# Kernel optimization log

Measured on AMD Instinct MI355X. Metric: run time of the kernel, lower is better.

## Reference

```python
import jax, jax.numpy as jnp
import numpy as np

B, L, D = 2, 2048, 1024
H = 16
HD = D // H  # 64


def _orthogonal_projection(key, d, m):
    g = jax.random.normal(key, (d, m), dtype=jnp.float32)
    q, r = jnp.linalg.qr(g)
    s = jnp.sign(jnp.diagonal(r))
    s = jnp.where(s == 0, 1.0, s)
    q = q * s[None, :]
    # preserve_variance=True
    return q * np.sqrt(d / m)


def setup_inputs() -> dict:
    key = jax.random.key(0)
    ks = jax.random.split(key, 8)
    x = jax.random.normal(ks[0], (B, L, D), dtype=jnp.float32)
    p = jax.random.normal(ks[1], (B, L, D), dtype=jnp.float32)
    s = 1.0 / np.sqrt(D)
    W_qkv = jax.random.uniform(ks[2], (3 * D, D), dtype=jnp.float32, minval=-s, maxval=s)
    b_qkv = jax.random.uniform(ks[3], (3 * D,), dtype=jnp.float32, minval=-s, maxval=s)
    W_out = jax.random.uniform(ks[4], (D, D), dtype=jnp.float32, minval=-s, maxval=s)
    b_out = jax.random.uniform(ks[5], (D,), dtype=jnp.float32, minval=-s, maxval=s)
    proj = _orthogonal_projection(ks[6], D, D // 2)
    return {"x": x, "p": p, "W_qkv": W_qkv, "b_qkv": b_qkv,
            "W_out": W_out, "b_out": b_out, "proj": proj}


def reference(x, p, W_qkv, b_qkv, W_out, b_out, proj):
    # QKV projection: (B,L,D) -> (B,L,3,H,HD)
    qkv = (jnp.einsum('bld,ed->ble', x, W_qkv) + b_qkv).reshape(B, L, 3, H, HD)
    q, k, v = qkv[:, :, 0], qkv[:, :, 1], qkv[:, :, 2]

    # Collaborative rotary phases from conditioning tokens: (B,L,H,HD/2)
    phases = (p @ proj).reshape(B, L, H, HD // 2)  # phase_scale = 1.0
    cos, sin = jnp.cos(phases), jnp.sin(phases)

    half = HD // 2
    # non-interleaved rotary: split head_dim into two halves
    def rot(t):
        t1, t2 = t[..., :half], t[..., half:]
        return jnp.concatenate([t1 * cos - t2 * sin, t1 * sin + t2 * cos], axis=-1)

    q, k = rot(q), rot(k)

    scale = HD ** -0.5
    scores = jnp.einsum('bqhd,bkhd->bhqk', q, k) * scale
    attn = jax.nn.softmax(scores, axis=-1)
    out = jnp.einsum('bhqk,bkhd->bqhd', attn, v).reshape(B, L, D)
    return jnp.einsum('bld,ed->ble', out, W_out) + b_out
```

## Files before the change

### kernel.cpp

```cpp
#include <hip/hip_runtime.h>
#include <hip/hip_bf16.h>
#include <math.h>

namespace {
constexpr int Bb = 2;
constexpr int Ll = 2048;
constexpr int Dd = 1024;
constexpr int Hh = 16;
constexpr int NT = Bb * Ll;
constexpr int D3 = 3 * Dd;
constexpr int PH = Dd / 2;
constexpr int LDK = 72;
}

typedef __attribute__((ext_vector_type(8))) short bf16x8;
typedef __attribute__((ext_vector_type(4))) float f32x4;

__device__ inline unsigned pack2bf(float a, float b) {
  __hip_bfloat162 t = __float22bfloat162_rn(float2{a, b});
  union { __hip_bfloat162 h; unsigned u; } cv; cv.h = t;
  return cv.u;
}

__device__ inline float bfhalf(unsigned u, int hi) {
  union { unsigned u; float f; } c;
  c.u = hi ? (u & 0xffff0000u) : (u << 16);
  return c.f;
}

__device__ inline void async_cp16(const void* gsrc, void* ldst) {
  __builtin_amdgcn_global_load_lds(
      (const __attribute__((address_space(1))) unsigned int*)gsrc,
      (__attribute__((address_space(3))) unsigned int*)ldst, 16, 0, 0);
}

__global__ __launch_bounds__(256) void prep_kernel(
    const float4* __restrict__ p, uint2* __restrict__ p_hi4, uint2* __restrict__ p_lo4,
    const float* __restrict__ proj, short* __restrict__ th, short* __restrict__ tl,
    const float4* __restrict__ x, const float4* __restrict__ wq, const float4* __restrict__ wo,
    uint2* __restrict__ xd, uint2* __restrict__ wqd, uint2* __restrict__ wod)
{
  __shared__ float Ls[64][65];
  const int bid = blockIdx.x;
  const int tid = threadIdx.x;

  if (bid < 4096) {
    const int i = bid * 256 + tid;
    const float4 f = p[i];
    float hf[4], lf[4];
    const float ff[4] = {f.x, f.y, f.z, f.w};
#pragma unroll
    for (int j = 0; j < 4; ++j) {
      const __hip_bfloat16 h = __float2bfloat16(ff[j]);
      hf[j] = __bfloat162float(h);
      lf[j] = ff[j] - hf[j];
    }
    p_hi4[i] = make_uint2(pack2bf(hf[0], hf[1]), pack2bf(hf[2], hf[3]));
    p_lo4[i] = make_uint2(pack2bf(lf[0], lf[1]), pack2bf(lf[2], lf[3]));
  } else if (bid < 4224) {
    const int bx = bid - 4096;
    const int d0 = (bx & 15) * 64, m0 = (bx >> 4) * 64;
    const int r = tid >> 4, c4 = (tid & 15) * 4;
#pragma unroll
    for (int it = 0; it < 4; ++it) {
      const int row = it * 16 + r;
      const float4 v = *(const float4*)&proj[(size_t)(d0 + row) * PH + m0 + c4];
      Ls[row][c4] = v.x; Ls[row][c4+1] = v.y; Ls[row][c4+2] = v.z; Ls[row][c4+3] = v.w;
    }
    __syncthreads();
#pragma unroll
    for (int it = 0; it < 4; ++it) {
      const int row = it * 16 + r;
      float hf[4], lf[4];
#pragma unroll
      for (int j = 0; j < 4; ++j) {
        const float v = Ls[c4 + j][row];
        const __hip_bfloat16 h = __float2bfloat16(v);
        hf[j] = __bfloat162float(h);
        lf[j] = v - hf[j];
      }
      *(uint2*)&th[(size_t)(m0 + row) * Dd + d0 + c4] = make_uint2(pack2bf(hf[0], hf[1]), pack2bf(hf[2], hf[3]));
      *(uint2*)&tl[(size_t)(m0 + row) * Dd + d0 + c4] = make_uint2(pack2bf(lf[0], lf[1]), pack2bf(lf[2], lf[3]));
    }
  } else {
    int i = (bid - 4224) * 256 + tid;
    const float4* s; uint2* d;
    if (i < 1048576) { s = x; d = xd; }
    else if (i < 1048576 + 786432) { i -= 1048576; s = wq; d = wqd; }
    else { i -= 1048576 + 786432; s = wo; d = wod; }
    const float4 f = s[i];
    d[i] = make_uint2(pack2bf(f.x, f.y), pack2bf(f.z, f.w));
  }
}

__global__ __launch_bounds__(256) void gemm_nn_split(
    const short* __restrict__ Ah_g, const short* __restrict__ Al_g,
    const short* __restrict__ Wh_g, const short* __restrict__ Wl_g,
    float* __restrict__ C)
{
  __shared__ __align__(16) short Ah[64 * 32], Al[64 * 32], Wh[64 * 32], Wl[64 * 32];
  const int tid = threadIdx.x;
  const int w = tid >> 6, lane = tid & 63;
  const int l15 = lane & 15, quad = lane >> 4;
  const int n0 = blockIdx.y * 64, m0 = blockIdx.x * 64;

  const int row = tid >> 2, cc = tid & 3;
  const int ksw = (cc ^ (row & 3)) * 8;
  const short* gAh = Ah_g + (size_t)(n0 + row) * Dd + ksw;
  const short* gAl = Al_g + (size_t)(n0 + row) * Dd + ksw;
  const short* gWh = Wh_g + (size_t)(m0 + row) * Dd + ksw;
  const short* gWl = Wl_g + (size_t)(m0 + row) * Dd + ksw;
  short* lAh = Ah + tid * 8;
  short* lAl = Al + tid * 8;
  short* lWh = Wh + tid * 8;
  short* lWl = Wl + tid * 8;

  f32x4 acc[4];
#pragma unroll
  for (int j = 0; j < 4; ++j) acc[j] = f32x4{0.f, 0.f, 0.f, 0.f};

  const int swq = (quad ^ (l15 & 3)) * 8;

  for (int k0 = 0; k0 < Dd; k0 += 32) {
    __syncthreads();
    async_cp16(gAh + k0, lAh);
    async_cp16(gAl + k0, lAl);
    async_cp16(gWh + k0, lWh);
    async_cp16(gWl + k0, lWl);
    __syncthreads();

    bf16x8 ah, al, wh[4], wl[4];
    ah = *(const bf16x8*)&Ah[(w * 16 + l15) * 32 + swq];
    al = *(const bf16x8*)&Al[(w * 16 + l15) * 32 + swq];
#pragma unroll
    for (int j = 0; j < 4; ++j) {
      wh[j] = *(const bf16x8*)&Wh[(j * 16 + l15) * 32 + swq];
      wl[j] = *(const bf16x8*)&Wl[(j * 16 + l15) * 32 + swq];
    }
#pragma unroll
    for (int j = 0; j < 4; ++j) {
      acc[j] = __builtin_amdgcn_mfma_f32_16x16x32_bf16(ah, wh[j], acc[j], 0, 0, 0);
      acc[j] = __builtin_amdgcn_mfma_f32_16x16x32_bf16(ah, wl[j], acc[j], 0, 0, 0);
      acc[j] = __builtin_amdgcn_mfma_f32_16x16x32_bf16(al, wh[j], acc[j], 0, 0, 0);
    }
  }

#pragma unroll
  for (int r = 0; r < 4; ++r) {
    float* crow = C + (size_t)(n0 + w * 16 + quad * 4 + r) * PH + m0 + l15;
#pragma unroll
    for (int j = 0; j < 4; ++j) crow[j * 16] = acc[j][r];
  }
}

__global__ __launch_bounds__(256) void gemm_qkv_fused(
    const __hip_bfloat16* __restrict__ A, const __hip_bfloat16* __restrict__ W,
    const float* __restrict__ bias, const float* __restrict__ phases,
    __hip_bfloat16* __restrict__ q_bf, __hip_bfloat16* __restrict__ k_bf,
    __hip_bfloat16* __restrict__ vt_g)
{
  __shared__ __align__(16) short As[128 * 32];
  __shared__ __align__(16) short Ws[128 * 32];
  const int tid = threadIdx.x;
  const int w = tid >> 6, lane = tid & 63;
  const int l15 = lane & 15, quad = lane >> 4;
  const int wn = w >> 1, wm = w & 1;
  const int n0 = blockIdx.y * 128, m0 = blockIdx.x * 128;

  const int row = tid >> 2, cc = tid & 3;
  const int ksw = (cc ^ (row & 3)) * 8;
  const short* gA  = (const short*)A + (size_t)(n0 + row) * Dd + ksw;
  const short* gW  = (const short*)W + (size_t)(m0 + row) * Dd + ksw;
  short* lA  = As + tid * 8;
  short* lA2 = As + 2048 + tid * 8;
  short* lW  = Ws + tid * 8;
  short* lW2 = Ws + 2048 + tid * 8;

  f32x4 acc[4][4];
#pragma unroll
  for (int i = 0; i < 4; ++i)
#pragma unroll
    for (int j = 0; j < 4; ++j) acc[i][j] = f32x4{0.f, 0.f, 0.f, 0.f};

  const int swq = (quad ^ (l15 & 3)) * 8;

  for (int k0 = 0; k0 < Dd; k0 += 32) {
    __syncthreads();
    async_cp16(gA + k0, lA);
    async_cp16(gA + 64 * Dd + k0, lA2);
    async_cp16(gW + k0, lW);
    async_cp16(gW + 64 * Dd + k0, lW2);
    __syncthreads();

    bf16x8 af[4], bf[4];
#pragma unroll
    for (int i = 0; i < 4; ++i)
      af[i] = *(const bf16x8*)&As[(wn * 64 + i * 16 + l15) * 32 + swq];
#pragma unroll
    for (int j = 0; j < 4; ++j)
      bf[j] = *(const bf16x8*)&Ws[(wm * 64 + j * 16 + l15) * 32 + swq];
#pragma unroll
    for (int i = 0; i < 4; ++i)
#pragma unroll
      for (int j = 0; j < 4; ++j)
        acc[i][j] = __builtin_amdgcn_mfma_f32_16x16x32_bf16(af[i], bf[j], acc[i][j], 0, 0, 0);
  }

  float bv[4];
#pragma unroll
  for (int j = 0; j < 4; ++j) bv[j] = bias[m0 + wm * 64 + j * 16 + l15];

  const int region = m0 >> 10;
  const int mloc = (m0 & 1023) + wm * 64;
  const int h = mloc >> 6;

  if (region < 2) {
    __hip_bfloat16* dst = region == 0 ? q_bf : k_bf;
    const float SC = region == 0 ? 0.18033688011112042f : 1.0f;
#pragma unroll
    for (int i = 0; i < 4; ++i)
#pragma unroll
      for (int r = 0; r < 4; ++r) {
        const int n = n0 + wn * 64 + i * 16 + quad * 4 + r;
        const float* phrow = phases + (size_t)n * PH + h * 32;
        __hip_bfloat16* drow = dst + (size_t)n * Dd + h * 64;
#pragma unroll
        for (int pz = 0; pz < 2; ++pz) {
          const float ph = phrow[pz * 16 + l15];
          float sn, cs;
          __sincosf(ph, &sn, &cs);
          const float a1 = acc[i][pz][r] + bv[pz];
          const float a2 = acc[i][pz + 2][r] + bv[pz + 2];
          drow[pz * 16 + l15]      = __float2bfloat16((a1 * cs - a2 * sn) * SC);
          drow[pz * 16 + 32 + l15] = __float2bfloat16((a1 * sn + a2 * cs) * SC);
        }
      }
  } else {
    const int bh = (n0 >> 11) * 16 + h;
    const int tokb = (n0 & 2047) + wn * 64;
#pragma unroll
    for (int i = 0; i < 4; ++i)
#pragma unroll
      for (int j = 0; j < 4; ++j) {
        const uint2 o = make_uint2(
            pack2bf(acc[i][j][0] + bv[j], acc[i][j][1] + bv[j]),
            pack2bf(acc[i][j][2] + bv[j], acc[i][j][3] + bv[j]));
        const int d = j * 16 + l15;
        *(uint2*)&vt_g[(size_t)(bh * 64 + d) * Ll + tokb + i * 16 + quad * 4] = o;
      }
  }
}

__global__ __launch_bounds__(256) void gemm_bt_64(
    const __hip_bfloat16* __restrict__ A, const __hip_bfloat16* __restrict__ W,
    const float* __restrict__ bias, float* __restrict__ C, int K, int M)
{
  __shared__ __align__(16) short As[128 * 32];
  __shared__ __align__(16) short Ws[64 * 32];
  const int tid = threadIdx.x;
  const int w = tid >> 6, lane = tid & 63;
  const int l15 = lane & 15, quad = lane >> 4;
  const int n0 = blockIdx.y * 128, m0 = blockIdx.x * 64;

  const int row = tid >> 2, cc = tid & 3;
  const int ksw = (cc ^ (row & 3)) * 8;
  const short* gA = (const short*)A + (size_t)(n0 + row) * K + ksw;
  const short* gW = (const short*)W + (size_t)(m0 + row) * K + ksw;
  short* lA  = As + tid * 8;
  short* lA2 = As + 2048 + tid * 8;
  short* lW  = Ws + tid * 8;

  f32x4 acc[2][4];
#pragma unroll
  for (int i = 0; i < 2; ++i)
#pragma unroll
    for (int j = 0; j < 4; ++j) acc[i][j] = f32x4{0.f, 0.f, 0.f, 0.f};

  const int swq = (quad ^ (l15 & 3)) * 8;

  for (int k0 = 0; k0 < K; k0 += 32) {
    __syncthreads();
    async_cp16(gA + k0, lA);
    async_cp16(gA + 64 * K + k0, lA2);
    async_cp16(gW + k0, lW);
    __syncthreads();

    bf16x8 af[2], bf[4];
#pragma unroll
    for (int i = 0; i < 2; ++i)
      af[i] = *(const bf16x8*)&As[(w * 32 + i * 16 + l15) * 32 + swq];
#pragma unroll
    for (int j = 0; j < 4; ++j)
      bf[j] = *(const bf16x8*)&Ws[(j * 16 + l15) * 32 + swq];
#pragma unroll
    for (int i = 0; i < 2; ++i)
#pragma unroll
      for (int j = 0; j < 4; ++j)
        acc[i][j] = __builtin_amdgcn_mfma_f32_16x16x32_bf16(af[i], bf[j], acc[i][j], 0, 0, 0);
  }

  float bv[4];
#pragma unroll
  for (int j = 0; j < 4; ++j) bv[j] = bias[m0 + j * 16 + l15];
#pragma unroll
  for (int i = 0; i < 2; ++i)
#pragma unroll
    for (int r = 0; r < 4; ++r) {
      float* crow = C + (size_t)(n0 + w * 32 + i * 16 + quad * 4 + r) * M + m0 + l15;
#pragma unroll
      for (int j = 0; j < 4; ++j) crow[j * 16] = acc[i][j][r] + bv[j];
    }
}

__global__ __launch_bounds__(256) void attn_mfma(
    const __hip_bfloat16* __restrict__ q_bf,
    const __hip_bfloat16* __restrict__ k_bf,
    const __hip_bfloat16* __restrict__ vt_g,
    __hip_bfloat16* __restrict__ o_part,
    float* __restrict__ lden_g)
{
  __shared__ __align__(16) short Ks[64 * LDK];
  __shared__ __align__(16) short Vt[64 * LDK];

  const int tid = threadIdx.x;
  const int w = tid >> 6;
  const int lane = tid & 63;
  const int l15 = lane & 15;
  const int quad = lane >> 4;

  const int q0 = blockIdx.x * 128;
  const int bh = blockIdx.y;
  const int kz = blockIdx.z;
  const int b = bh >> 4, h = bh & 15;
  const int kt0 = kz * 16;

  bf16x8 qfrag[2][2];
#pragma unroll
  for (int qg = 0; qg < 2; ++qg)
#pragma unroll
    for (int kh = 0; kh < 2; ++kh) {
      const size_t qrow = (size_t)(b * Ll + q0 + w * 32 + qg * 16 + l15);
      qfrag[qg][kh] = *(const bf16x8*)(q_bf + qrow * Dd + h * 64 + kh * 32 + quad * 8);
    }

  f32x4 acc[4][2];
#pragma unroll
  for (int dt = 0; dt < 4; ++dt)
#pragma unroll
    for (int qg = 0; qg < 2; ++qg) acc[dt][qg] = f32x4{0.f, 0.f, 0.f, 0.f};
  f32x4 lden[2] = {f32x4{0.f,0.f,0.f,0.f}, f32x4{0.f,0.f,0.f,0.f}};
  const short one_bf = (short)0x3F80;
  const bf16x8 ones8 = {one_bf, one_bf, one_bf, one_bf, one_bf, one_bf, one_bf, one_bf};

  const int srow = tid >> 2, sseg = tid & 3;
  const __hip_bfloat16* kbase = k_bf + (size_t)(b * Ll + srow) * Dd + h * 64 + sseg * 16;
  const __hip_bfloat16* vbase = vt_g + ((size_t)(bh * 64 + srow)) * Ll + sseg * 16;

  uint4 pk0, pk1, pv0, pv1;
  {
    const uint4* kg = (const uint4*)(kbase + (size_t)kt0 * 64 * Dd);
    pk0 = kg[0]; pk1 = kg[1];
    const uint4* vg = (const uint4*)(vbase + kt0 * 64);
    pv0 = vg[0]; pv1 = vg[1];
  }

  for (int kt = 0; kt < 16; ++kt) {
    __syncthreads();
    *(uint4*)&Ks[srow * LDK + sseg * 16]     = pk0;
    *(uint4*)&Ks[srow * LDK + sseg * 16 + 8] = pk1;
    *(uint4*)&Vt[srow * LDK + sseg * 16]     = pv0;
    *(uint4*)&Vt[srow * LDK + sseg * 16 + 8] = pv1;
    __syncthreads();

    {
      const int ktn = kt0 + ((kt + 1) & 15);
      const uint4* kg = (const uint4*)(kbase + (size_t)ktn * 64 * Dd);
      pk0 = kg[0]; pk1 = kg[1];
      const uint4* vg = (const uint4*)(vbase + ktn * 64);
      pv0 = vg[0]; pv1 = vg[1];
    }

    f32x4 s[4][2];
#pragma unroll
    for (int n = 0; n < 4; ++n)
#pragma unroll
      for (int qg = 0; qg < 2; ++qg) s[n][qg] = f32x4{0.f, 0.f, 0.f, 0.f};
#pragma unroll
    for (int n = 0; n < 4; ++n)
#pragma unroll
      for (int kh = 0; kh < 2; ++kh) {
        const bf16x8 af = *(const bf16x8*)&Ks[(n * 16 + l15) * LDK + kh * 32 + quad * 8];
        s[n][0] = __builtin_amdgcn_mfma_f32_16x16x32_bf16(af, qfrag[0][kh], s[n][0], 0, 0, 0);
        s[n][1] = __builtin_amdgcn_mfma_f32_16x16x32_bf16(af, qfrag[1][kh], s[n][1], 0, 0, 0);
      }

    uint2 bq[4][2];
#pragma unroll
    for (int qg = 0; qg < 2; ++qg)
#pragma unroll
      for (int n = 0; n < 4; ++n) {
        union { float f; unsigned u; } p0, p1, p2, p3;
        p0.f = __builtin_amdgcn_exp2f(s[n][qg][0]);
        p1.f = __builtin_amdgcn_exp2f(s[n][qg][1]);
        p2.f = __builtin_amdgcn_exp2f(s[n][qg][2]);
        p3.f = __builtin_amdgcn_exp2f(s[n][qg][3]);
        bq[n][qg] = make_uint2(__builtin_amdgcn_perm(p1.u, p0.u, 0x07060302u),
                               __builtin_amdgcn_perm(p3.u, p2.u, 0x07060302u));
      }

#pragma unroll
    for (int pr = 0; pr < 2; ++pr) {
      bf16x8 va[4];
#pragma unroll
      for (int dt = 0; dt < 4; ++dt)
        va[dt] = *(const bf16x8*)&Vt[(dt * 16 + l15) * LDK + pr * 32 + quad * 8];
#pragma unroll
      for (int qg = 0; qg < 2; ++qg) {
        const uint2 a = bq[2 * pr][qg];
        const uint2 c = bq[2 * pr + 1][qg];
        auto rx32 = __builtin_amdgcn_permlane32_swap(a.x, c.x, false, false);
        auto rx16 = __builtin_amdgcn_permlane16_swap(rx32[0], rx32[1], false, false);
        auto ry32 = __builtin_amdgcn_permlane32_swap(a.y, c.y, false, false);
        auto ry16 = __builtin_amdgcn_permlane16_swap(ry32[0], ry32[1], false, false);
        union { unsigned u[4]; bf16x8 v; } pb;
        pb.u[0] = rx16[0]; pb.u[1] = ry16[0]; pb.u[2] = rx16[1]; pb.u[3] = ry16[1];
        lden[qg] = __builtin_amdgcn_mfma_f32_16x16x32_bf16(ones8, pb.v, lden[qg], 0, 0, 0);
#pragma unroll
        for (int dt = 0; dt < 4; ++dt)
          acc[dt][qg] = __builtin_amdgcn_mfma_f32_16x16x32_bf16(va[dt], pb.v, acc[dt][qg], 0, 0, 0);
      }
    }
  }

#pragma unroll
  for (int qg = 0; qg < 2; ++qg) {
    const float lv = lden[qg][0];
    const float linv = 1.f / lv;
    const int ql = q0 + w * 32 + qg * 16 + l15;
    if (quad == 0)
      lden_g[((size_t)(kz * Bb + b) * Hh + h) * Ll + ql] = lv;
    __hip_bfloat16* dst = o_part + ((size_t)kz * NT + b * Ll + ql) * Dd + h * 64;
#pragma unroll
    for (int dt = 0; dt < 4; ++dt) {
      const uint2 o = make_uint2(
          pack2bf(acc[dt][qg][0] * linv, acc[dt][qg][1] * linv),
          pack2bf(acc[dt][qg][2] * linv, acc[dt][qg][3] * linv));
      *(uint2*)&dst[dt * 16 + quad * 4] = o;
    }
  }
}

__global__ __launch_bounds__(256) void attn_combine(
    const __hip_bfloat16* __restrict__ o_part, const float* __restrict__ lden_g,
    __hip_bfloat16* __restrict__ aout)
{
  const int i = blockIdx.x * 256 + threadIdx.x;
  const int n = i >> 8, d4 = i & 255;
  const int b = n >> 11, l = n & 2047;
  const int h = d4 >> 4;
  const float l0 = lden_g[((size_t)b * Hh + h) * Ll + l];
  const float l1 = lden_g[((size_t)(Bb + b) * Hh + h) * Ll + l];
  const float inv = 1.f / (l0 + l1);
  const float w0 = l0 * inv, w1 = l1 * inv;
  const uint2 a0 = ((const uint2*)o_part)[i];
  const uint2 a1 = ((const uint2*)o_part)[(NT * (size_t)Dd / 4) + i];
  const float r0 = w0 * bfhalf(a0.x, 0) + w1 * bfhalf(a1.x, 0);
  const float r1 = w0 * bfhalf(a0.x, 1) + w1 * bfhalf(a1.x, 1);
  const float r2 = w0 * bfhalf(a0.y, 0) + w1 * bfhalf(a1.y, 0);
  const float r3 = w0 * bfhalf(a0.y, 1) + w1 * bfhalf(a1.y, 1);
  ((uint2*)aout)[i] = make_uint2(pack2bf(r0, r1), pack2bf(r2, r3));
}

extern "C" void kernel_launch(void* const* d_in, const int* in_sizes, int n_in,
                              void* d_out, int out_size, void* d_ws, size_t ws_size,
                              hipStream_t stream) {
  const float* x     = (const float*)d_in[0];
  const float* p     = (const float*)d_in[1];
  const float* W_qkv = (const float*)d_in[2];
  const float* b_qkv = (const float*)d_in[3];
  const float* W_out = (const float*)d_in[4];
  const float* b_out = (const float*)d_in[5];
  const float* proj  = (const float*)d_in[6];
  float* out = (float*)d_out;

  char* wsb = (char*)d_ws;
  float*          phases   = (float*)(wsb);
  short*          p_hi     = (short*)(wsb + (8u << 20));
  __hip_bfloat16* aout_bf  = (__hip_bfloat16*)(wsb + (8u << 20));
  short*          p_lo     = (short*)(wsb + (16u << 20));
  __hip_bfloat16* vt_g     = (__hip_bfloat16*)(wsb + (16u << 20));
  short*          projt_hi = (short*)(wsb + (24u << 20));
  short*          projt_lo = (short*)(wsb + (25u << 20));
  __hip_bfloat16* q_bf     = (__hip_bfloat16*)(wsb + (26u << 20));
  __hip_bfloat16* k_bf     = (__hip_bfloat16*)(wsb + (34u << 20));
  __hip_bfloat16* x_bf     = (__hip_bfloat16*)(wsb + (42u << 20));
  __hip_bfloat16* o_part   = (__hip_bfloat16*)(wsb + (42u << 20));
  __hip_bfloat16* wqkv_bf  = (__hip_bfloat16*)(wsb + (50u << 20));
  __hip_bfloat16* wout_bf  = (__hip_bfloat16*)(wsb + (58u << 20));
  float*          lden_g   = (float*)(wsb + (60u << 20));

  prep_kernel<<<12416, 256, 0, stream>>>(
      (const float4*)p, (uint2*)p_hi, (uint2*)p_lo,
      proj, projt_hi, projt_lo,
      (const float4*)x, (const float4*)W_qkv, (const float4*)W_out,
      (uint2*)x_bf, (uint2*)wqkv_bf, (uint2*)wout_bf);
  gemm_nn_split<<<dim3(PH / 64, NT / 64), 256, 0, stream>>>(p_hi, p_lo, projt_hi, projt_lo, phases);
  gemm_qkv_fused<<<dim3(D3 / 128, NT / 128), 256, 0, stream>>>(x_bf, wqkv_bf, b_qkv, phases,
                                                               q_bf, k_bf, vt_g);
  attn_mfma<<<dim3(Ll / 128, Bb * Hh, 2), 256, 0, stream>>>(q_bf, k_bf, vt_g, o_part, lden_g);
  attn_combine<<<4096, 256, 0, stream>>>(o_part, lden_g, aout_bf);
  gemm_bt_64<<<dim3(Dd / 64, NT / 128), 256, 0, stream>>>(aout_bf, wout_bf, b_out, out, Dd, Dd);
}
```

Measured before the change: 252.7 us.

## Double-buffer attention K/V tiles with async LDS copies and pre-swizzled layout

The QKV epilogue now writes K and V^T to global memory with an XOR swizzle on the column index. The attention kernel can then copy 16-byte chunks straight into LDS with async copies, replacing the register-staged, padded LDS stores. K/V tiles are double-buffered, so the next tile loads while the current one is computed, and only one barrier per iteration is needed instead of two. s_setprio is raised around the MFMA clusters to favour matrix issue. The risks are hidden wait-count correctness for the async copies and the coupling between the producer-side swizzle and the consumer-side indexing.

```diff
diff --git a/kernel.cpp b/kernel.cpp
--- a/kernel.cpp
+++ b/kernel.cpp
@@ -10,7 +10,6 @@
 constexpr int NT = Bb * Ll;
 constexpr int D3 = 3 * Dd;
 constexpr int PH = Dd / 2;
-constexpr int LDK = 72;
 }
 
 typedef __attribute__((ext_vector_type(8))) short bf16x8;
@@ -217,11 +216,13 @@
   if (region < 2) {
     __hip_bfloat16* dst = region == 0 ? q_bf : k_bf;
     const float SC = region == 0 ? 0.18033688011112042f : 1.0f;
+    const int dosw = (region == 1);
 #pragma unroll
     for (int i = 0; i < 4; ++i)
 #pragma unroll
       for (int r = 0; r < 4; ++r) {
         const int n = n0 + wn * 64 + i * 16 + quad * 4 + r;
+        const int swz = dosw ? (((quad * 4 + r) & 7) << 3) : 0;
         const float* phrow = phases + (size_t)n * PH + h * 32;
         __hip_bfloat16* drow = dst + (size_t)n * Dd + h * 64;
 #pragma unroll
@@ -231,13 +232,14 @@
           __sincosf(ph, &sn, &cs);
           const float a1 = acc[i][pz][r] + bv[pz];
           const float a2 = acc[i][pz + 2][r] + bv[pz + 2];
-          drow[pz * 16 + l15]      = __float2bfloat16((a1 * cs - a2 * sn) * SC);
-          drow[pz * 16 + 32 + l15] = __float2bfloat16((a1 * sn + a2 * cs) * SC);
+          drow[(pz * 16 + l15) ^ swz]      = __float2bfloat16((a1 * cs - a2 * sn) * SC);
+          drow[(pz * 16 + 32 + l15) ^ swz] = __float2bfloat16((a1 * sn + a2 * cs) * SC);
         }
       }
   } else {
     const int bh = (n0 >> 11) * 16 + h;
     const int tokb = (n0 & 2047) + wn * 64;
+    const int vsw = (l15 & 7) << 3;
 #pragma unroll
     for (int i = 0; i < 4; ++i)
 #pragma unroll
@@ -246,7 +248,7 @@
             pack2bf(acc[i][j][0] + bv[j], acc[i][j][1] + bv[j]),
             pack2bf(acc[i][j][2] + bv[j], acc[i][j][3] + bv[j]));
         const int d = j * 16 + l15;
-        *(uint2*)&vt_g[(size_t)(bh * 64 + d) * Ll + tokb + i * 16 + quad * 4] = o;
+        *(uint2*)&vt_g[(size_t)(bh * 64 + d) * Ll + tokb + ((i * 16 + quad * 4) ^ vsw)] = o;
       }
   }
 }
@@ -319,8 +321,7 @@
     __hip_bfloat16* __restrict__ o_part,
     float* __restrict__ lden_g)
 {
-  __shared__ __align__(16) short Ks[64 * LDK];
-  __shared__ __align__(16) short Vt[64 * LDK];
+  __shared__ __align__(16) short KV[2][2][4096];
 
   const int tid = threadIdx.x;
   const int w = tid >> 6;
@@ -352,47 +353,55 @@
   const short one_bf = (short)0x3F80;
   const bf16x8 ones8 = {one_bf, one_bf, one_bf, one_bf, one_bf, one_bf, one_bf, one_bf};
 
-  const int srow = tid >> 2, sseg = tid & 3;
-  const __hip_bfloat16* kbase = k_bf + (size_t)(b * Ll + srow) * Dd + h * 64 + sseg * 16;
-  const __hip_bfloat16* vbase = vt_g + ((size_t)(bh * 64 + srow)) * Ll + sseg * 16;
-
-  uint4 pk0, pk1, pv0, pv1;
+  const __hip_bfloat16* ksrc = k_bf + ((size_t)(b * Ll) + (tid >> 3)) * Dd + h * 64 + (tid & 7) * 8;
+  const __hip_bfloat16* vsrc = vt_g + ((size_t)(bh * 64) + (tid >> 3)) * Ll + (tid & 7) * 8;
+  const int ldst = tid * 8;
+
+  const int sw = (l15 & 7) << 3;
+  const int co0 = (quad * 8) ^ sw;
+  const int co1 = (32 + quad * 8) ^ sw;
+
   {
-    const uint4* kg = (const uint4*)(kbase + (size_t)kt0 * 64 * Dd);
-    pk0 = kg[0]; pk1 = kg[1];
-    const uint4* vg = (const uint4*)(vbase + kt0 * 64);
-    pv0 = vg[0]; pv1 = vg[1];
+    const __hip_bfloat16* kp = ksrc + (size_t)kt0 * 64 * Dd;
+    const __hip_bfloat16* vp = vsrc + (size_t)kt0 * 64;
+    async_cp16(kp,                    &KV[0][0][ldst]);
+    async_cp16(kp + (size_t)32 * Dd,  &KV[0][0][2048 + ldst]);
+    async_cp16(vp,                    &KV[0][1][ldst]);
+    async_cp16(vp + (size_t)32 * Ll,  &KV[0][1][2048 + ldst]);
   }
 
   for (int kt = 0; kt < 16; ++kt) {
     __syncthreads();
-    *(uint4*)&Ks[srow * LDK + sseg * 16]     = pk0;
-    *(uint4*)&Ks[srow * LDK + sseg * 16 + 8] = pk1;
-    *(uint4*)&Vt[srow * LDK + sseg * 16]     = pv0;
-    *(uint4*)&Vt[srow * LDK + sseg * 16 + 8] = pv1;
-    __syncthreads();
-
-    {
-      const int ktn = kt0 + ((kt + 1) & 15);
-      const uint4* kg = (const uint4*)(kbase + (size_t)ktn * 64 * Dd);
-      pk0 = kg[0]; pk1 = kg[1];
-      const uint4* vg = (const uint4*)(vbase + ktn * 64);
-      pv0 = vg[0]; pv1 = vg[1];
-    }
+    const int cur = kt & 1;
+    if (kt + 1 < 16) {
+      const int ktn = kt0 + kt + 1;
+      const __hip_bfloat16* kp = ksrc + (size_t)ktn * 64 * Dd;
+      const __hip_bfloat16* vp = vsrc + (size_t)ktn * 64;
+      async_cp16(kp,                    &KV[cur ^ 1][0][ldst]);
+      async_cp16(kp + (size_t)32 * Dd,  &KV[cur ^ 1][0][2048 + ldst]);
+      async_cp16(vp,                    &KV[cur ^ 1][1][ldst]);
+      async_cp16(vp + (size_t)32 * Ll,  &KV[cur ^ 1][1][2048 + ldst]);
+    }
+    const short* Ks = &KV[cur][0][0];
+    const short* Vt = &KV[cur][1][0];
 
     f32x4 s[4][2];
 #pragma unroll
     for (int n = 0; n < 4; ++n)
 #pragma unroll
       for (int qg = 0; qg < 2; ++qg) s[n][qg] = f32x4{0.f, 0.f, 0.f, 0.f};
-#pragma unroll
-    for (int n = 0; n < 4; ++n)
-#pragma unroll
-      for (int kh = 0; kh < 2; ++kh) {
-        const bf16x8 af = *(const bf16x8*)&Ks[(n * 16 + l15) * LDK + kh * 32 + quad * 8];
-        s[n][0] = __builtin_amdgcn_mfma_f32_16x16x32_bf16(af, qfrag[0][kh], s[n][0], 0, 0, 0);
-        s[n][1] = __builtin_amdgcn_mfma_f32_16x16x32_bf16(af, qfrag[1][kh], s[n][1], 0, 0, 0);
-      }
+
+    __builtin_amdgcn_s_setprio(1);
+#pragma unroll
+    for (int n = 0; n < 4; ++n) {
+      const bf16x8 af0 = *(const bf16x8*)&Ks[(n * 16 + l15) * 64 + co0];
+      const bf16x8 af1 = *(const bf16x8*)&Ks[(n * 16 + l15) * 64 + co1];
+      s[n][0] = __builtin_amdgcn_mfma_f32_16x16x32_bf16(af0, qfrag[0][0], s[n][0], 0, 0, 0);
+      s[n][1] = __builtin_amdgcn_mfma_f32_16x16x32_bf16(af0, qfrag[1][0], s[n][1], 0, 0, 0);
+      s[n][0] = __builtin_amdgcn_mfma_f32_16x16x32_bf16(af1, qfrag[0][1], s[n][0], 0, 0, 0);
+      s[n][1] = __builtin_amdgcn_mfma_f32_16x16x32_bf16(af1, qfrag[1][1], s[n][1], 0, 0, 0);
+    }
+    __builtin_amdgcn_s_setprio(0);
 
     uint2 bq[4][2];
 #pragma unroll
@@ -410,10 +419,11 @@
 
 #pragma unroll
     for (int pr = 0; pr < 2; ++pr) {
+      const int cop = pr ? co1 : co0;
       bf16x8 va[4];
 #pragma unroll
       for (int dt = 0; dt < 4; ++dt)
-        va[dt] = *(const bf16x8*)&Vt[(dt * 16 + l15) * LDK + pr * 32 + quad * 8];
+        va[dt] = *(const bf16x8*)&Vt[(dt * 16 + l15) * 64 + cop];
 #pragma unroll
       for (int qg = 0; qg < 2; ++qg) {
         const uint2 a = bq[2 * pr][qg];
@@ -424,10 +434,12 @@
         auto ry16 = __builtin_amdgcn_permlane16_swap(ry32[0], ry32[1], false, false);
         union { unsigned u[4]; bf16x8 v; } pb;
         pb.u[0] = rx16[0]; pb.u[1] = ry16[0]; pb.u[2] = rx16[1]; pb.u[3] = ry16[1];
+        __builtin_amdgcn_s_setprio(1);
         lden[qg] = __builtin_amdgcn_mfma_f32_16x16x32_bf16(ones8, pb.v, lden[qg], 0, 0, 0);
 #pragma unroll
         for (int dt = 0; dt < 4; ++dt)
           acc[dt][qg] = __builtin_amdgcn_mfma_f32_16x16x32_bf16(va[dt], pb.v, acc[dt][qg], 0, 0, 0);
+        __builtin_amdgcn_s_setprio(0);
       }
     }
   }
```

Result: no change. 251.3 us (-0.6%).
